# Kernel optimization log

Hardware: AMD Instinct MI355X
Metric: run time of the kernel (lower is better)

## Reference

```python
import jax, jax.numpy as jnp
import numpy as np

B, N, C, D, O = 32, 512, 16, 256, 256


def setup_inputs() -> dict:
    key = jax.random.key(0)
    k1, k2, k3, k4, k5, k6 = jax.random.split(key, 6)
    std = 1.0 / np.sqrt(D)
    nodes = jax.random.normal(k1, (B, N, D), jnp.float32)
    children = jax.random.randint(k2, (B, N, C), 0, N)  # 0 == no-child sentinel
    w_t = jax.random.normal(k3, (D, O), jnp.float32) * std
    w_l = jax.random.normal(k4, (D, O), jnp.float32) * std
    w_r = jax.random.normal(k5, (D, O), jnp.float32) * std
    conv = jax.random.normal(k6, (O,), jnp.float32) * np.sqrt(2.0 / D)
    return {"nodes": nodes, "w_t": w_t, "w_l": w_l, "w_r": w_r, "conv": conv,
            "children": children}


def _coefs(children):
    # children: (B, N, C) int. Returns coef (B, N, C+1, 3) = stack(c_t, c_r, c_l).
    b, n, c = children.shape
    y = c + 1
    has_child = jnp.minimum(children, 1).astype(jnp.float32)          # (B,N,C)
    mask = jnp.concatenate([jnp.zeros((b, n, 1), jnp.float32), has_child], axis=2)  # (B,N,Y)
    # eta_t: 1 at slot 0 (parent), 0 elsewhere
    c_t = jnp.concatenate([jnp.ones((b, n, 1), jnp.float32),
                           jnp.zeros((b, n, c), jnp.float32)], axis=2)
    # eta_r
    ns = jnp.count_nonzero(children, axis=2).astype(jnp.float32)[..., None]  # (B,N,1)
    p = jnp.arange(-1.0, c, dtype=jnp.float32)                        # (Y,): -1,0,1,...
    child_idx = p * mask                                              # (B,N,Y)
    singles = (jnp.arange(y) == 1).astype(jnp.float32) * 0.5          # (Y,)
    denom = jnp.where(ns == 1.0, 1.0, ns - 1.0)                       # safe divide
    c_r = jnp.where(ns == 1.0,
                    jnp.broadcast_to(singles, mask.shape),
                    (1.0 - c_t) * (child_idx / denom))
    # eta_l
    c_l = (1.0 - c_t) * (1.0 - c_r) * mask
    return jnp.stack([c_t, c_r, c_l], axis=3)                         # (B,N,Y,3)


def reference(nodes, w_t, w_l, w_r, conv, children):
    b, n, d = nodes.shape
    c = children.shape[2]
    # gather children embeddings: child_emb[b,i,j] = nodes[b, children[b,i,j]]
    flat_idx = children.reshape(b, n * c)
    child_emb = jnp.take_along_axis(nodes, flat_idx[:, :, None], axis=1)
    child_emb = child_emb.reshape(b, n, c, d)
    child_emb = jnp.where((children == 0)[..., None], 0.0, child_emb)
    tree = jnp.concatenate([nodes[:, :, None, :], child_emb], axis=2)  # (B,N,Y,D)
    coef = _coefs(children)                                            # (B,N,Y,3)
    weights = jnp.stack([w_t, w_r, w_l], axis=0)                       # (3,D,O)
    agg = jnp.einsum('bnyd,bnyk->bnkd', tree, coef)                    # (B,N,3,D)
    res = jnp.einsum('bnkd,kdo->bno', agg, weights)                    # (B,N,O)
    return jax.nn.leaky_relu(res + conv, negative_slope=0.01)
```

## Files before the change

### kernel.cpp

```cpp
#include <hip/hip_runtime.h>
#include <hip/hip_bf16.h>
#include <stdint.h>

#define BB 32
#define NNODE 512
#define CC 16
#define DD 256
#define OO 256
#define K3 768
#define TM 32
#define NSLAB 24
#define ASTR 776

typedef __attribute__((ext_vector_type(8))) short bf16x8;
typedef __attribute__((ext_vector_type(4))) float f32x4;

__device__ __forceinline__ unsigned short f2bf(float x) {
    unsigned u = __builtin_bit_cast(unsigned, x);
    u += 0x7FFFu + ((u >> 16) & 1u);
    return (unsigned short)(u >> 16);
}

__device__ __forceinline__ void st_bf4(unsigned short* p, float4 v) {
    uint2 u;
    u.x = (unsigned)f2bf(v.x) | ((unsigned)f2bf(v.y) << 16);
    u.y = (unsigned)f2bf(v.z) | ((unsigned)f2bf(v.w) << 16);
    *(uint2*)p = u;
}

__global__ void prep_w(const float* __restrict__ wt,
                       const float* __restrict__ wr,
                       const float* __restrict__ wl,
                       unsigned short* __restrict__ wsb) {
    __shared__ unsigned short T[256 * 40];
    const int slab = blockIdx.x;
    const int n = threadIdx.x;
#pragma unroll
    for (int kk = 0; kk < 32; ++kk) {
        const int k = slab * 32 + kk;
        const float* s = (k < 256) ? wt : ((k < 512) ? wr : wl);
        T[n * 40 + kk] = f2bf(s[(k & 255) * OO + n]);
    }
    __syncthreads();
    uint4* dst = (uint4*)(wsb + slab * 8192 + n * 32);
    const uint4* src = (const uint4*)&T[n * 40];
#pragma unroll
    for (int q = 0; q < 4; ++q) dst[q] = src[q];
}

__global__ __launch_bounds__(512, 4) void tbcnn_main(
    const float* __restrict__ nodes, const int* __restrict__ children,
    const unsigned short* __restrict__ wsb, const float* __restrict__ conv,
    float* __restrict__ out) {

    __shared__ unsigned short Atile[TM * ASTR];

    const int tid  = threadIdx.x;
    const int wave = tid >> 6;
    const int lane = tid & 63;
    const int p  = blockIdx.x;
    const int lb = (p & 7) * 64 + (p >> 3);
    const int base = lb * TM;
    const float4* gnodes4 = (const float4*)nodes;

#pragma unroll 1
    for (int i = 0; i < 4; ++i) {
        const int m  = wave * 4 + i;
        const int nf = base + m;
        const int brow = (nf >> 9) << 9;
        const int4* ch4 = (const int4*)(children + (nf << 4));
        int4 c0 = ch4[0], c1 = ch4[1], c2 = ch4[2], c3 = ch4[3];
        int cj[CC] = {c0.x, c0.y, c0.z, c0.w, c1.x, c1.y, c1.z, c1.w,
                      c2.x, c2.y, c2.z, c2.w, c3.x, c3.y, c3.z, c3.w};
        int ns = 0;
#pragma unroll
        for (int j = 0; j < CC; ++j) ns += (cj[j] != 0) ? 1 : 0;
        const float inv_den = (ns > 1) ? 1.0f / (float)(ns - 1) : 0.0f;
        const bool single = (ns == 1);

        float4 pt = gnodes4[(size_t)nf * 64 + lane];
        float4 ar = make_float4(0.f, 0.f, 0.f, 0.f);
        float4 al = make_float4(0.f, 0.f, 0.f, 0.f);
#pragma unroll
        for (int j = 0; j < CC; ++j) {
            const int idx = cj[j];
            const float hasf = (idx != 0) ? 1.0f : 0.0f;
            float4 e = gnodes4[((size_t)(brow + idx)) * 64 + lane];
            const float crr_raw = single ? ((j == 0) ? 0.5f : 0.0f)
                                         : (float)j * inv_den * hasf;
            const float cr = crr_raw * hasf;
            const float cl = (1.0f - crr_raw) * hasf;
            ar.x += cr * e.x; ar.y += cr * e.y; ar.z += cr * e.z; ar.w += cr * e.w;
            al.x += cl * e.x; al.y += cl * e.y; al.z += cl * e.z; al.w += cl * e.w;
        }
        unsigned short* arow = &Atile[m * ASTR];
        st_bf4(arow + 0   + lane * 4, pt);
        st_bf4(arow + 256 + lane * 4, ar);
        st_bf4(arow + 512 + lane * 4, al);
    }
    __syncthreads();

    const int wr = wave >> 2;
    const int wc = wave & 3;
    const int quad = lane >> 4;
    const int l16  = lane & 15;
    f32x4 acc[4];
#pragma unroll
    for (int ni = 0; ni < 4; ++ni) acc[ni] = (f32x4){0.f, 0.f, 0.f, 0.f};

#pragma unroll 2
    for (int s = 0; s < NSLAB; ++s) {
        bf16x8 a = *(const bf16x8*)&Atile[(wr * 16 + l16) * ASTR + s * 32 + quad * 8];
#pragma unroll
        for (int ni = 0; ni < 4; ++ni) {
            bf16x8 b = *(const bf16x8*)(wsb + s * 8192
                                        + (wc * 64 + ni * 16 + l16) * 32 + quad * 8);
            acc[ni] = __builtin_amdgcn_mfma_f32_16x16x32_bf16(a, b, acc[ni], 0, 0, 0);
        }
    }

#pragma unroll
    for (int ni = 0; ni < 4; ++ni) {
        const int o = wc * 64 + ni * 16 + l16;
        const float cv = conv[o];
#pragma unroll
        for (int r = 0; r < 4; ++r) {
            const int row = base + wr * 16 + quad * 4 + r;
            float v = acc[ni][r] + cv;
            v = (v > 0.f) ? v : 0.01f * v;
            out[(size_t)row * OO + o] = v;
        }
    }
}

extern "C" void kernel_launch(void* const* d_in, const int* in_sizes, int n_in,
                              void* d_out, int out_size, void* d_ws, size_t ws_size,
                              hipStream_t stream) {
    const float* nodes    = (const float*)d_in[0];
    const float* w_t      = (const float*)d_in[1];
    const float* w_l      = (const float*)d_in[2];
    const float* w_r      = (const float*)d_in[3];
    const float* conv     = (const float*)d_in[4];
    const int*   children = (const int*)d_in[5];

    unsigned short* wsb = (unsigned short*)d_ws;

    prep_w<<<24, 256, 0, stream>>>(w_t, w_r, w_l, wsb);
    tbcnn_main<<<512, 512, 0, stream>>>(nodes, children, wsb, conv, (float*)d_out);
}
```

Measured before the change: 115.0 us.

## Split gather into separate kernel and double-buffered LDS GEMM via global_load_lds

Replaces the fused gather+GEMM kernel with two kernels. The first does the child gather and coefficient aggregation into a bf16 workspace laid out in pre-tiled slabs, and folds the weight conversion into the same launch. The second runs a 64x128-tile MFMA GEMM that streams A and B slabs into double-buffered LDS with async global_load_lds. The goal is to decouple latency-bound gathers from the GEMM and give the matmul more reuse and overlap, at the cost of writing and re-reading a ~25MB intermediate in global memory.

```diff
diff --git a/kernel.cpp b/kernel.cpp
--- a/kernel.cpp
+++ b/kernel.cpp
@@ -2,15 +2,14 @@
 #include <hip/hip_bf16.h>
 #include <stdint.h>
 
-#define BB 32
-#define NNODE 512
 #define CC 16
-#define DD 256
 #define OO 256
-#define K3 768
-#define TM 32
 #define NSLAB 24
-#define ASTR 776
+#define MT_ROWS 64
+#define SLAB_ELS (MT_ROWS * 32)
+#define MT_ELS (NSLAB * SLAB_ELS)
+#define AGG_ELS (16384 * 768)
+#define NGB 2048
 
 typedef __attribute__((ext_vector_type(8))) short bf16x8;
 typedef __attribute__((ext_vector_type(4))) float f32x4;
@@ -28,46 +27,49 @@
     *(uint2*)p = u;
 }
 
-__global__ void prep_w(const float* __restrict__ wt,
-                       const float* __restrict__ wr,
-                       const float* __restrict__ wl,
-                       unsigned short* __restrict__ wsb) {
+__device__ __forceinline__ void cp16(const void* g, void* l) {
+    __builtin_amdgcn_global_load_lds(
+        (const __attribute__((address_space(1))) unsigned int*)g,
+        (__attribute__((address_space(3))) unsigned int*)l, 16, 0, 0);
+}
+
+__global__ __launch_bounds__(256, 4) void gather_prep(
+    const float* __restrict__ nodes, const int* __restrict__ children,
+    const float* __restrict__ wt, const float* __restrict__ wrp,
+    const float* __restrict__ wl, unsigned short* __restrict__ agg,
+    unsigned short* __restrict__ wsb) {
+
     __shared__ unsigned short T[256 * 40];
-    const int slab = blockIdx.x;
-    const int n = threadIdx.x;
-#pragma unroll
-    for (int kk = 0; kk < 32; ++kk) {
-        const int k = slab * 32 + kk;
-        const float* s = (k < 256) ? wt : ((k < 512) ? wr : wl);
-        T[n * 40 + kk] = f2bf(s[(k & 255) * OO + n]);
-    }
-    __syncthreads();
-    uint4* dst = (uint4*)(wsb + slab * 8192 + n * 32);
-    const uint4* src = (const uint4*)&T[n * 40];
-#pragma unroll
-    for (int q = 0; q < 4; ++q) dst[q] = src[q];
-}
-
-__global__ __launch_bounds__(512, 4) void tbcnn_main(
-    const float* __restrict__ nodes, const int* __restrict__ children,
-    const unsigned short* __restrict__ wsb, const float* __restrict__ conv,
-    float* __restrict__ out) {
-
-    __shared__ unsigned short Atile[TM * ASTR];
-
-    const int tid  = threadIdx.x;
+    const int p = blockIdx.x;
+    const int tid = threadIdx.x;
+
+    if (p >= NGB) {
+        const int slab = p - NGB;
+        const int n = tid;
+#pragma unroll
+        for (int kk = 0; kk < 32; ++kk) {
+            const int k = slab * 32 + kk;
+            const float* s = (k < 256) ? wt : ((k < 512) ? wrp : wl);
+            T[n * 40 + kk] = f2bf(s[(k & 255) * OO + n]);
+        }
+        __syncthreads();
+        uint4* dst = (uint4*)(wsb + slab * 8192 + n * 32);
+        const uint4* src = (const uint4*)&T[n * 40];
+#pragma unroll
+        for (int q = 0; q < 4; ++q) dst[q] = src[q];
+        return;
+    }
+
     const int wave = tid >> 6;
     const int lane = tid & 63;
-    const int p  = blockIdx.x;
-    const int lb = (p & 7) * 64 + (p >> 3);
-    const int base = lb * TM;
-    const float4* gnodes4 = (const float4*)nodes;
-
-#pragma unroll 1
-    for (int i = 0; i < 4; ++i) {
-        const int m  = wave * 4 + i;
-        const int nf = base + m;
-        const int brow = (nf >> 9) << 9;
+    const int lb = (p & 7) * 256 + (p >> 3);
+    const int base = lb * 8;
+    const float4* g4 = (const float4*)nodes;
+
+#pragma unroll
+    for (int i = 0; i < 2; ++i) {
+        const int nf = base + wave * 2 + i;
+        const int brow = nf & ~511;
         const int4* ch4 = (const int4*)(children + (nf << 4));
         int4 c0 = ch4[0], c1 = ch4[1], c2 = ch4[2], c3 = ch4[3];
         int cj[CC] = {c0.x, c0.y, c0.z, c0.w, c1.x, c1.y, c1.z, c1.w,
@@ -78,57 +80,103 @@
         const float inv_den = (ns > 1) ? 1.0f / (float)(ns - 1) : 0.0f;
         const bool single = (ns == 1);
 
-        float4 pt = gnodes4[(size_t)nf * 64 + lane];
+        float4 pt = g4[(size_t)nf * 64 + lane];
         float4 ar = make_float4(0.f, 0.f, 0.f, 0.f);
         float4 al = make_float4(0.f, 0.f, 0.f, 0.f);
 #pragma unroll
         for (int j = 0; j < CC; ++j) {
             const int idx = cj[j];
             const float hasf = (idx != 0) ? 1.0f : 0.0f;
-            float4 e = gnodes4[((size_t)(brow + idx)) * 64 + lane];
+            float4 e = g4[((size_t)(brow + idx)) * 64 + lane];
             const float crr_raw = single ? ((j == 0) ? 0.5f : 0.0f)
-                                         : (float)j * inv_den * hasf;
+                                         : (float)j * inv_den;
             const float cr = crr_raw * hasf;
             const float cl = (1.0f - crr_raw) * hasf;
             ar.x += cr * e.x; ar.y += cr * e.y; ar.z += cr * e.z; ar.w += cr * e.w;
             al.x += cl * e.x; al.y += cl * e.y; al.z += cl * e.z; al.w += cl * e.w;
         }
-        unsigned short* arow = &Atile[m * ASTR];
-        st_bf4(arow + 0   + lane * 4, pt);
-        st_bf4(arow + 256 + lane * 4, ar);
-        st_bf4(arow + 512 + lane * 4, al);
-    }
-    __syncthreads();
-
-    const int wr = wave >> 2;
-    const int wc = wave & 3;
+        const int sl = lane >> 3;
+        const int kw = (lane & 7) * 4;
+        unsigned short* rowp = agg + (size_t)(nf >> 6) * MT_ELS
+                                   + (size_t)(nf & 63) * 32 + kw;
+        st_bf4(rowp + (size_t)(0  + sl) * SLAB_ELS, pt);
+        st_bf4(rowp + (size_t)(8  + sl) * SLAB_ELS, ar);
+        st_bf4(rowp + (size_t)(16 + sl) * SLAB_ELS, al);
+    }
+}
+
+__global__ __launch_bounds__(256, 2) void gemm_ep(
+    const unsigned short* __restrict__ agg, const unsigned short* __restrict__ wsb,
+    const float* __restrict__ conv, float* __restrict__ out) {
+
+    __shared__ unsigned short Ab[2][SLAB_ELS];
+    __shared__ unsigned short Bb[2][4096];
+
+    const int tid  = threadIdx.x;
+    const int wave = tid >> 6;
+    const int lane = tid & 63;
     const int quad = lane >> 4;
     const int l16  = lane & 15;
-    f32x4 acc[4];
-#pragma unroll
-    for (int ni = 0; ni < 4; ++ni) acc[ni] = (f32x4){0.f, 0.f, 0.f, 0.f};
-
-#pragma unroll 2
+    const int mtile = blockIdx.x >> 1;
+    const int ntile = blockIdx.x & 1;
+    const int wrr = wave >> 1;
+    const int wcc = wave & 1;
+
+    const char* aggb = (const char*)agg + (size_t)mtile * (MT_ELS * 2);
+    const char* wsbb = (const char*)wsb + ntile * 8192;
+    const int toff  = tid * 16;
+    const int wbase = (tid & ~63) * 16;
+
+    f32x4 acc[2][4];
+#pragma unroll
+    for (int mi = 0; mi < 2; ++mi)
+#pragma unroll
+        for (int ni = 0; ni < 4; ++ni)
+            acc[mi][ni] = (f32x4){0.f, 0.f, 0.f, 0.f};
+
+    auto stage = [&](int s, int b) {
+        const char* ga = aggb + s * 4096 + toff;
+        cp16(ga, (char*)&Ab[b][0] + wbase);
+        const char* gb = wsbb + s * 16384 + toff;
+        cp16(gb,        (char*)&Bb[b][0] + wbase);
+        cp16(gb + 4096, (char*)&Bb[b][0] + wbase + 4096);
+    };
+
+    stage(0, 0);
+#pragma unroll 1
     for (int s = 0; s < NSLAB; ++s) {
-        bf16x8 a = *(const bf16x8*)&Atile[(wr * 16 + l16) * ASTR + s * 32 + quad * 8];
-#pragma unroll
-        for (int ni = 0; ni < 4; ++ni) {
-            bf16x8 b = *(const bf16x8*)(wsb + s * 8192
-                                        + (wc * 64 + ni * 16 + l16) * 32 + quad * 8);
-            acc[ni] = __builtin_amdgcn_mfma_f32_16x16x32_bf16(a, b, acc[ni], 0, 0, 0);
-        }
+        const int cur = s & 1;
+        __syncthreads();
+        if (s + 1 < NSLAB) stage(s + 1, cur ^ 1);
+
+        bf16x8 af[2], bfr[4];
+#pragma unroll
+        for (int mi = 0; mi < 2; ++mi)
+            af[mi] = *(const bf16x8*)&Ab[cur][(wrr * 32 + mi * 16 + l16) * 32 + quad * 8];
+#pragma unroll
+        for (int ni = 0; ni < 4; ++ni)
+            bfr[ni] = *(const bf16x8*)&Bb[cur][(wcc * 64 + ni * 16 + l16) * 32 + quad * 8];
+#pragma unroll
+        for (int mi = 0; mi < 2; ++mi)
+#pragma unroll
+            for (int ni = 0; ni < 4; ++ni)
+                acc[mi][ni] = __builtin_amdgcn_mfma_f32_16x16x32_bf16(
+                    af[mi], bfr[ni], acc[mi][ni], 0, 0, 0);
     }
 
 #pragma unroll
     for (int ni = 0; ni < 4; ++ni) {
-        const int o = wc * 64 + ni * 16 + l16;
-        const float cv = conv[o];
-#pragma unroll
-        for (int r = 0; r < 4; ++r) {
-            const int row = base + wr * 16 + quad * 4 + r;
-            float v = acc[ni][r] + cv;
-            v = (v > 0.f) ? v : 0.01f * v;
-            out[(size_t)row * OO + o] = v;
+        const int col = ntile * 128 + wcc * 64 + ni * 16 + l16;
+        const float cv = conv[col];
+#pragma unroll
+        for (int mi = 0; mi < 2; ++mi) {
+#pragma unroll
+            for (int r = 0; r < 4; ++r) {
+                const int row = mtile * 64 + wrr * 32 + mi * 16 + quad * 4 + r;
+                float v = acc[mi][ni][r] + cv;
+                v = (v > 0.f) ? v : 0.01f * v;
+                out[(size_t)row * OO + col] = v;
+            }
         }
     }
 }
@@ -143,8 +191,10 @@
     const float* conv     = (const float*)d_in[4];
     const int*   children = (const int*)d_in[5];
 
-    unsigned short* wsb = (unsigned short*)d_ws;
-
-    prep_w<<<24, 256, 0, stream>>>(w_t, w_r, w_l, wsb);
-    tbcnn_main<<<512, 512, 0, stream>>>(nodes, children, wsb, conv, (float*)d_out);
-}
+    unsigned short* agg = (unsigned short*)d_ws;
+    unsigned short* wsb = agg + AGG_ELS;
+
+    gather_prep<<<NGB + 24, 256, 0, stream>>>(nodes, children, w_t, w_r, w_l,
+                                              agg, wsb);
+    gemm_ep<<<512, 256, 0, stream>>>(agg, wsb, conv, (float*)d_out);
+}
```

Result: faster. 107.0 us (-7.0%).
